# Kernel optimization log

Hardware: AMD Instinct MI355X
Metric: run time of the kernel (lower is better)

Reference implementation:

```python
import jax, jax.numpy as jnp
import numpy as np

NUM_HEADS = 16

def phi(x):
    return jax.nn.elu(x) + 1.0

def setup_inputs() -> dict:
    key = jax.random.key(0)
    ks = jax.random.split(key, 8)
    B, Tq, Tk, H = 4, 8192, 8192, 1024
    s = 1.0 / np.sqrt(H)
    return {
        "q": jax.random.normal(ks[0], (B, Tq, H), jnp.float32),
        "k": jax.random.normal(ks[1], (B, Tk, H), jnp.float32),
        "v": jax.random.normal(ks[2], (B, Tk, H), jnp.float32),
        "mask": jnp.ones((B, Tk), jnp.float32),
        "Wq": jax.random.normal(ks[3], (H, H), jnp.float32) * s,
        "Wk": jax.random.normal(ks[4], (H, H), jnp.float32) * s,
        "Wv": jax.random.normal(ks[5], (H, H), jnp.float32) * s,
        "Wo": jax.random.normal(ks[6], (H, H), jnp.float32) * s,
    }

def reference(q, k, v, mask, Wq, Wk, Wv, Wo):
    B, Tq, H = q.shape
    Tk = k.shape[1]
    nh = NUM_HEADS
    d = H // nh
    # projections (torch Linear: x @ W.T), split heads -> bhtd
    Q = (q @ Wq.T).reshape(B, Tq, nh, d).transpose(0, 2, 1, 3)
    K = (k @ Wk.T).reshape(B, Tk, nh, d).transpose(0, 2, 1, 3)
    V = (v @ Wv.T).reshape(B, Tk, nh, d).transpose(0, 2, 1, 3)
    Q = phi(Q)
    K = phi(K)
    m = mask[:, None, :, None]  # b1t1
    K = K * m
    V = V * m
    K_sum = K.sum(axis=2)                          # bhd
    KV = jnp.einsum('bhtd,bhtv->bhdv', K, V)       # bh d d
    Z = 1.0 / (jnp.einsum('bhtd,bhd->bht', Q, K_sum) + 1e-6)
    out = jnp.einsum('bhtd,bhdv->bhtv', Q, KV) * Z[..., None]
    out = out.transpose(0, 2, 1, 3).reshape(B, Tq, H)
    return out @ Wo.T
```

## Files before the change

### kernel.cpp

```cpp
#include <hip/hip_runtime.h>
#include <hip/hip_bf16.h>
#include <stdint.h>

#define B_  4
#define T_  8192
#define H_  1024
#define NH_ 16
#define D_  64
#define BT_ (B_*T_)

typedef __attribute__((ext_vector_type(8))) __bf16 bf16x8;
typedef __attribute__((ext_vector_type(4))) __bf16 bf16x4;
typedef __attribute__((ext_vector_type(4))) float  f32x4;

__device__ __forceinline__ float phi_f(float x) {
    return x > 0.0f ? x + 1.0f : __expf(x);
}

__device__ __forceinline__ void async_copy16(const void* g, void* l) {
    __builtin_amdgcn_global_load_lds(
        (const __attribute__((address_space(1))) uint32_t*)g,
        (__attribute__((address_space(3))) uint32_t*)l, 16, 0, 0);
}

__global__ void conv_bf16(const float* __restrict__ src, __bf16* __restrict__ dst) {
    size_t i = ((size_t)blockIdx.x * 256 + threadIdx.x) * 8;
    float4 a = *(const float4*)(src + i);
    float4 b = *(const float4*)(src + i + 4);
    bf16x8 o;
    o[0]=(__bf16)a.x; o[1]=(__bf16)a.y; o[2]=(__bf16)a.z; o[3]=(__bf16)a.w;
    o[4]=(__bf16)b.x; o[5]=(__bf16)b.y; o[6]=(__bf16)b.z; o[7]=(__bf16)b.w;
    *(bf16x8*)(dst + i) = o;
}

__global__ void wconv4(const float* __restrict__ s0, const float* __restrict__ s1,
                       const float* __restrict__ s2, const float* __restrict__ s3,
                       __bf16* __restrict__ d0, __bf16* __restrict__ d1,
                       __bf16* __restrict__ d2, __bf16* __restrict__ d3) {
    const float* s; __bf16* d;
    switch (blockIdx.y) {
        case 0: s = s0; d = d0; break;
        case 1: s = s1; d = d1; break;
        case 2: s = s2; d = d2; break;
        default: s = s3; d = d3; break;
    }
    int i = (blockIdx.x * 256 + threadIdx.x) * 4;
    float4 v = *(const float4*)(s + i);
    bf16x4 o;
    o[0] = (__bf16)v.x; o[1] = (__bf16)v.y; o[2] = (__bf16)v.z; o[3] = (__bf16)v.w;
    *(bf16x4*)(d + i) = o;
}

template<int EPI>
__global__ __launch_bounds__(256, 2)
void gemm_bt(const __bf16* __restrict__ A, const __bf16* __restrict__ Wb,
             const float* __restrict__ mask, void* __restrict__ OutV)
{
    const int orig = blockIdx.x;
    const int wgid = (orig & 7) * 256 + (orig >> 3);
    const int bm = (wgid >> 3) * 128;
    const int bn = (wgid & 7) * 128;
    const int tid  = threadIdx.x;
    const int lane = tid & 63;
    const int wid  = tid >> 6;
    const int wm = wid >> 1, wn = wid & 1;

    __shared__ __bf16 Al[128 * 64];
    __shared__ __bf16 Bl[128 * 64];

    f32x4 acc[4][4];
    #pragma unroll
    for (int i = 0; i < 4; ++i)
        #pragma unroll
        for (int j = 0; j < 4; ++j) acc[i][j] = (f32x4)0.0f;

    const int sn = wid * 8 + (lane >> 3);
    const int sc = (lane & 7) * 16;

    for (int k0 = 0; k0 < H_; k0 += 64) {
        #pragma unroll
        for (int issue = 0; issue < 4; ++issue) {
            int n = issue * 32 + sn;
            int csw = sc ^ ((n & 7) << 4);
            async_copy16((const char*)(A  + (size_t)(bm + n) * H_ + k0) + csw,
                         (char*)Al + issue * 4096 + wid * 1024);
            async_copy16((const char*)(Wb + (size_t)(bn + n) * H_ + k0) + csw,
                         (char*)Bl + issue * 4096 + wid * 1024);
        }
        __syncthreads();
        #pragma unroll
        for (int ks = 0; ks < 2; ++ks) {
            bf16x8 afr[4], bfr[4];
            #pragma unroll
            for (int mi = 0; mi < 4; ++mi) {
                int r  = wm * 64 + mi * 16 + (lane & 15);
                int cb = (ks * 64 + (lane >> 4) * 16) ^ ((r & 7) << 4);
                afr[mi] = *(const bf16x8*)((const char*)Al + r * 128 + cb);
            }
            #pragma unroll
            for (int ni = 0; ni < 4; ++ni) {
                int r  = wn * 64 + ni * 16 + (lane & 15);
                int cb = (ks * 64 + (lane >> 4) * 16) ^ ((r & 7) << 4);
                bfr[ni] = *(const bf16x8*)((const char*)Bl + r * 128 + cb);
            }
            #pragma unroll
            for (int mi = 0; mi < 4; ++mi)
                #pragma unroll
                for (int ni = 0; ni < 4; ++ni)
                    acc[mi][ni] = __builtin_amdgcn_mfma_f32_16x16x32_bf16(
                        afr[mi], bfr[ni], acc[mi][ni], 0, 0, 0);
        }
        __syncthreads();
    }
    const int gm0 = bm + wm * 64;
    const int gn0 = bn + wn * 64 + (lane & 15);
    #pragma unroll
    for (int mi = 0; mi < 4; ++mi) {
        #pragma unroll
        for (int j = 0; j < 4; ++j) {
            int gm = gm0 + mi * 16 + (lane >> 4) * 4 + j;
            if (EPI == 3) {
                float* op = (float*)OutV + (size_t)gm * H_ + gn0;
                #pragma unroll
                for (int ni = 0; ni < 4; ++ni)
                    op[ni * 16] = acc[mi][ni][j];
            } else {
                float mv = (EPI >= 1) ? mask[gm] : 1.0f;
                __bf16* op = (__bf16*)OutV + (size_t)gm * H_ + gn0;
                #pragma unroll
                for (int ni = 0; ni < 4; ++ni) {
                    float v = acc[mi][ni][j];
                    if (EPI == 0)      v = phi_f(v);
                    else if (EPI == 1) v = phi_f(v) * mv;
                    else               v = v * mv;
                    op[ni * 16] = (__bf16)v;
                }
            }
        }
    }
}

__global__ __launch_bounds__(256, 2)
void kv_kernel(const __bf16* __restrict__ Kb, const __bf16* __restrict__ Vb,
               float* __restrict__ KVp, float* __restrict__ Ksp)
{
    const int chunk = blockIdx.x;
    const int bh = blockIdx.y;
    const int b = bh >> 4, h = bh & 15;
    const int tid = threadIdx.x, lane = tid & 63, wid = tid >> 6;

    __shared__ char KtRaw[64 * 144];
    __shared__ char VtRaw[64 * 144];
    __shared__ float ksbuf[32][64];

    const int st  = tid >> 3;
    const int dkg = tid & 7;
    const int dk0 = dkg * 8;
    const int swzT = (dkg & 7) << 4;

    f32x4 acc[4];
    #pragma unroll
    for (int i = 0; i < 4; ++i) acc[i] = (f32x4)0.0f;
    float ksacc[8];
    #pragma unroll
    for (int i = 0; i < 8; ++i) ksacc[i] = 0.0f;

    const size_t gbase = ((size_t)b * T_ + (size_t)chunk * 1024) * H_
                         + h * 64 + dk0;

    bf16x8 ka, kc, va, vc;
    {
        const __bf16* p  = Kb + gbase;
        const __bf16* pv = Vb + gbase;
        ka = *(const bf16x8*)(p  + (size_t)st * H_);
        kc = *(const bf16x8*)(p  + (size_t)(st + 32) * H_);
        va = *(const bf16x8*)(pv + (size_t)st * H_);
        vc = *(const bf16x8*)(pv + (size_t)(st + 32) * H_);
    }

    for (int tile = 0; tile < 16; ++tile) {
        __syncthreads();
        #pragma unroll
        for (int j = 0; j < 8; ++j) {
            int rowb = (dk0 + j) * 144;
            *(__bf16*)(KtRaw + ((rowb + 2*st)        ^ swzT)) = ka[j];
            *(__bf16*)(KtRaw + ((rowb + 2*(st + 32)) ^ swzT)) = kc[j];
            *(__bf16*)(VtRaw + ((rowb + 2*st)        ^ swzT)) = va[j];
            *(__bf16*)(VtRaw + ((rowb + 2*(st + 32)) ^ swzT)) = vc[j];
            ksacc[j] += (float)ka[j] + (float)kc[j];
        }
        if (tile < 15) {
            const __bf16* p  = Kb + gbase + (size_t)(tile + 1) * 64 * H_;
            const __bf16* pv = Vb + gbase + (size_t)(tile + 1) * 64 * H_;
            ka = *(const bf16x8*)(p  + (size_t)st * H_);
            kc = *(const bf16x8*)(p  + (size_t)(st + 32) * H_);
            va = *(const bf16x8*)(pv + (size_t)st * H_);
            vc = *(const bf16x8*)(pv + (size_t)(st + 32) * H_);
        }
        __syncthreads();
        #pragma unroll
        for (int ks = 0; ks < 2; ++ks) {
            int r = wid * 16 + (lane & 15);
            int cb = (r * 144 + (ks * 64 + (lane >> 4) * 16)) ^ (((r >> 3) & 7) << 4);
            bf16x8 af = *(const bf16x8*)(KtRaw + cb);
            #pragma unroll
            for (int ni = 0; ni < 4; ++ni) {
                int rv = ni * 16 + (lane & 15);
                int cv = (rv * 144 + (ks * 64 + (lane >> 4) * 16)) ^ (((rv >> 3) & 7) << 4);
                bf16x8 bf = *(const bf16x8*)(VtRaw + cv);
                acc[ni] = __builtin_amdgcn_mfma_f32_16x16x32_bf16(af, bf, acc[ni], 0, 0, 0);
            }
        }
    }

    float* kvp = KVp + ((size_t)chunk * 64 + bh) * 4096;
    #pragma unroll
    for (int ni = 0; ni < 4; ++ni)
        #pragma unroll
        for (int jj = 0; jj < 4; ++jj) {
            int dk = wid * 16 + (lane >> 4) * 4 + jj;
            int dv = ni * 16 + (lane & 15);
            kvp[dk * 64 + dv] = acc[ni][jj];
        }

    #pragma unroll
    for (int j = 0; j < 8; ++j)
        ksbuf[st][dk0 + j] = ksacc[j];
    __syncthreads();
    if (tid < 64) {
        float s = 0.0f;
        #pragma unroll 8
        for (int st2 = 0; st2 < 32; ++st2) s += ksbuf[st2][tid];
        Ksp[((size_t)chunk * 64 + bh) * 64 + tid] = s;
    }
}

__global__ void kvt_kernel(const float* __restrict__ KVp, const float* __restrict__ Ksp,
                           __bf16* __restrict__ KVT, float* __restrict__ Ks) {
    int bh = blockIdx.x, tid = threadIdx.x;
    __bf16* d = KVT + (size_t)bh * 4096;
    for (int i = tid; i < 4096; i += 256) {
        float s = 0.0f;
        #pragma unroll
        for (int c = 0; c < 8; ++c)
            s += KVp[((size_t)c * 64 + bh) * 4096 + i];
        int dk = i >> 6, dv = i & 63;
        d[dv * 64 + dk] = (__bf16)s;
    }
    if (tid < 64) {
        float s = 0.0f;
        #pragma unroll
        for (int c = 0; c < 8; ++c)
            s += Ksp[((size_t)c * 64 + bh) * 64 + tid];
        Ks[bh * 64 + tid] = s;
    }
}

__global__ __launch_bounds__(256, 2)
void attn_kernel(const __bf16* __restrict__ Qb, const __bf16* __restrict__ KVT,
                 const float* __restrict__ Ksum, __bf16* __restrict__ On)
{
    const int bh = blockIdx.y;
    const int b = bh >> 4, h = bh & 15;
    const int tc = blockIdx.x;
    const int tid = threadIdx.x, lane = tid & 63, wid = tid >> 6;
    __shared__ __bf16 kvl[64][72];
    __shared__ float dinv[256];

    {
        const int r = tid >> 2, part = tid & 3;
        const __bf16* src = KVT + (size_t)bh * 4096 + r * 64 + part * 16;
        *(bf16x8*)&kvl[r][part*16]     = *(const bf16x8*)src;
        *(bf16x8*)&kvl[r][part*16 + 8] = *(const bf16x8*)(src + 8);
    }
    {
        const int t = tc * 256 + tid;
        const __bf16* qp = Qb + ((size_t)b * T_ + t) * H_ + h * 64;
        const float* kp = Ksum + bh * 64;
        float s = 0.0f;
        #pragma unroll
        for (int i = 0; i < 8; ++i) {
            bf16x8 qv = *(const bf16x8*)(qp + i * 8);
            #pragma unroll
            for (int j = 0; j < 8; ++j) s += (float)qv[j] * kp[i*8 + j];
        }
        dinv[tid] = 1.0f / (s + 1e-6f);
    }
    __syncthreads();

    f32x4 acc[4][4];
    #pragma unroll
    for (int i = 0; i < 4; ++i)
        #pragma unroll
        for (int j = 0; j < 4; ++j) acc[i][j] = (f32x4)0.0f;

    const int t0 = tc * 256 + wid * 64;
    #pragma unroll
    for (int ks = 0; ks < 2; ++ks) {
        bf16x8 afr[4], bfr[4];
        #pragma unroll
        for (int mi = 0; mi < 4; ++mi) {
            int t = t0 + mi * 16 + (lane & 15);
            afr[mi] = *(const bf16x8*)(Qb + ((size_t)b * T_ + t) * H_ + h * 64
                                       + ks * 32 + (lane >> 4) * 8);
        }
        #pragma unroll
        for (int ni = 0; ni < 4; ++ni) {
            int dv = ni * 16 + (lane & 15);
            bfr[ni] = *(const bf16x8*)&kvl[dv][ks * 32 + (lane >> 4) * 8];
        }
        #pragma unroll
        for (int mi = 0; mi < 4; ++mi)
            #pragma unroll
            for (int ni = 0; ni < 4; ++ni)
                acc[mi][ni] = __builtin_amdgcn_mfma_f32_16x16x32_bf16(
                    afr[mi], bfr[ni], acc[mi][ni], 0, 0, 0);
    }
    #pragma unroll
    for (int mi = 0; mi < 4; ++mi)
        #pragma unroll
        for (int j = 0; j < 4; ++j) {
            int lt = wid * 64 + mi * 16 + (lane >> 4) * 4 + j;
            float z = dinv[lt];
            int t = tc * 256 + lt;
            __bf16* op = On + ((size_t)b * T_ + t) * H_ + h * 64 + (lane & 15);
            #pragma unroll
            for (int ni = 0; ni < 4; ++ni)
                op[ni * 16] = (__bf16)(acc[mi][ni][j] * z);
        }
}

extern "C" void kernel_launch(void* const* d_in, const int* in_sizes, int n_in,
                              void* d_out, int out_size, void* d_ws, size_t ws_size,
                              hipStream_t stream) {
    (void)in_sizes; (void)n_in; (void)out_size; (void)ws_size;
    const float* q    = (const float*)d_in[0];
    const float* k    = (const float*)d_in[1];
    const float* v    = (const float*)d_in[2];
    const float* mask = (const float*)d_in[3];
    const float* Wq   = (const float*)d_in[4];
    const float* Wk   = (const float*)d_in[5];
    const float* Wv   = (const float*)d_in[6];
    const float* Wo   = (const float*)d_in[7];
    float* out = (float*)d_out;

    char* ws = (char*)d_ws;
    const size_t WELEM = (size_t)H_ * H_;
    const size_t PELEM = (size_t)BT_ * H_;
    __bf16* Wqb = (__bf16*)ws;
    __bf16* Wkb = Wqb + WELEM;
    __bf16* Wvb = Wkb + WELEM;
    __bf16* Wob = Wvb + WELEM;
    __bf16* Qb  = Wob + WELEM;
    __bf16* Kb  = Qb + PELEM;
    __bf16* Vb  = Kb + PELEM;
    __bf16* tmp = Vb + PELEM;
    float*  KVp = (float*)(tmp + PELEM);
    float*  Ksp = KVp + (size_t)8 * 64 * 4096;
    float*  Ksf = Ksp + (size_t)8 * 64 * 64;
    __bf16* KVT = (__bf16*)(Ksf + (size_t)64 * 64);

    wconv4<<<dim3(1024, 4), 256, 0, stream>>>(Wq, Wk, Wv, Wo, Wqb, Wkb, Wvb, Wob);

    const int cgrid = (int)(PELEM / (256 * 8));
    conv_bf16<<<cgrid, 256, 0, stream>>>(q, tmp);
    gemm_bt<0><<<2048, 256, 0, stream>>>(tmp, Wqb, mask, Qb);
    conv_bf16<<<cgrid, 256, 0, stream>>>(k, tmp);
    gemm_bt<1><<<2048, 256, 0, stream>>>(tmp, Wkb, mask, Kb);
    conv_bf16<<<cgrid, 256, 0, stream>>>(v, tmp);
    gemm_bt<2><<<2048, 256, 0, stream>>>(tmp, Wvb, mask, Vb);

    kv_kernel<<<dim3(T_/1024, B_*NH_), 256, 0, stream>>>(Kb, Vb, KVp, Ksp);
    kvt_kernel<<<B_*NH_, 256, 0, stream>>>(KVp, Ksp, KVT, Ksf);
    attn_kernel<<<dim3(T_/256, B_*NH_), 256, 0, stream>>>(Qb, KVT, Ksf, tmp);
    gemm_bt<3><<<2048, 256, 0, stream>>>(tmp, Wob, mask, out);
}
```

Measured before the change: 460.7 us.

## Rewrite projection GEMM with 256x256 tiles and 4-stage async LDS pipeline

Replaces the 128x128-tile, single-buffered GEMM with a 256x256 tile using 512 threads (8 waves, each owning 128x64 outputs). A 4-deep ring of 32-wide K slices is staged into 128KB of LDS with direct global-to-LDS loads, and vmcnt-based waits with one barrier per step let loads overlap MFMA work. s_setprio is raised around the MFMA block. The aim is more data reuse per tile and hiding global memory latency, at the cost of large LDS and register use that limits occupancy. The new LDS layout drops the old XOR swizzle, which may bring bank conflicts.

```diff
diff --git a/kernel.cpp b/kernel.cpp
--- a/kernel.cpp
+++ b/kernel.cpp
@@ -52,70 +52,91 @@
 }
 
 template<int EPI>
-__global__ __launch_bounds__(256, 2)
+__global__ __launch_bounds__(512, 2)
 void gemm_bt(const __bf16* __restrict__ A, const __bf16* __restrict__ Wb,
              const float* __restrict__ mask, void* __restrict__ OutV)
 {
+    __shared__ __align__(16) char lds[131072];
+
     const int orig = blockIdx.x;
-    const int wgid = (orig & 7) * 256 + (orig >> 3);
-    const int bm = (wgid >> 3) * 128;
-    const int bn = (wgid & 7) * 128;
-    const int tid  = threadIdx.x;
+    const int wg = (orig & 7) * 64 + (orig >> 3);
+    const int bm = (wg >> 2) * 256;
+    const int bn = (wg & 3) * 256;
+    const int tid = threadIdx.x;
     const int lane = tid & 63;
-    const int wid  = tid >> 6;
-    const int wm = wid >> 1, wn = wid & 1;
-
-    __shared__ __bf16 Al[128 * 64];
-    __shared__ __bf16 Bl[128 * 64];
-
-    f32x4 acc[4][4];
-    #pragma unroll
-    for (int i = 0; i < 4; ++i)
+    const int w = tid >> 6;
+    const int wm = w >> 2, wn = w & 3;
+
+    const int sb0 = w * 1024 + lane * 16;
+    const int sb1 = sb0 + 8192;
+    const int kc0 = sb0 >> 12, row0 = (sb0 & 4095) >> 4;
+    const int kc1 = sb1 >> 12, row1 = (sb1 & 4095) >> 4;
+
+    const __bf16* a0 = A  + (size_t)(bm + row0) * H_ + kc0 * 8;
+    const __bf16* a1 = A  + (size_t)(bm + row1) * H_ + kc1 * 8;
+    const __bf16* b0 = Wb + (size_t)(bn + row0) * H_ + kc0 * 8;
+    const __bf16* b1 = Wb + (size_t)(bn + row1) * H_ + kc1 * 8;
+
+    const int ubA0 = w * 1024;
+    const int ubA1 = ubA0 + 8192;
+
+    const int aoff = (lane >> 4) * 4096 + (lane & 15) * 16 + wm * 2048;
+    const int boff = (lane >> 4) * 4096 + (lane & 15) * 16 + wn * 1024;
+
+    f32x4 acc[8][4];
+    #pragma unroll
+    for (int i = 0; i < 8; ++i)
         #pragma unroll
         for (int j = 0; j < 4; ++j) acc[i][j] = (f32x4)0.0f;
 
-    const int sn = wid * 8 + (lane >> 3);
-    const int sc = (lane & 7) * 16;
-
-    for (int k0 = 0; k0 < H_; k0 += 64) {
-        #pragma unroll
-        for (int issue = 0; issue < 4; ++issue) {
-            int n = issue * 32 + sn;
-            int csw = sc ^ ((n & 7) << 4);
-            async_copy16((const char*)(A  + (size_t)(bm + n) * H_ + k0) + csw,
-                         (char*)Al + issue * 4096 + wid * 1024);
-            async_copy16((const char*)(Wb + (size_t)(bn + n) * H_ + k0) + csw,
-                         (char*)Bl + issue * 4096 + wid * 1024);
-        }
-        __syncthreads();
-        #pragma unroll
-        for (int ks = 0; ks < 2; ++ks) {
-            bf16x8 afr[4], bfr[4];
-            #pragma unroll
-            for (int mi = 0; mi < 4; ++mi) {
-                int r  = wm * 64 + mi * 16 + (lane & 15);
-                int cb = (ks * 64 + (lane >> 4) * 16) ^ ((r & 7) << 4);
-                afr[mi] = *(const bf16x8*)((const char*)Al + r * 128 + cb);
-            }
-            #pragma unroll
-            for (int ni = 0; ni < 4; ++ni) {
-                int r  = wn * 64 + ni * 16 + (lane & 15);
-                int cb = (ks * 64 + (lane >> 4) * 16) ^ ((r & 7) << 4);
-                bfr[ni] = *(const bf16x8*)((const char*)Bl + r * 128 + cb);
-            }
-            #pragma unroll
-            for (int mi = 0; mi < 4; ++mi)
-                #pragma unroll
-                for (int ni = 0; ni < 4; ++ni)
-                    acc[mi][ni] = __builtin_amdgcn_mfma_f32_16x16x32_bf16(
-                        afr[mi], bfr[ni], acc[mi][ni], 0, 0, 0);
-        }
-        __syncthreads();
-    }
-    const int gm0 = bm + wm * 64;
+    auto STAGE = [&](int hh) {
+        const int s_ = (hh & 3) * 16384;
+        const int k_ = hh * 32;
+        async_copy16(a0 + k_, lds + s_ + ubA0);
+        async_copy16(a1 + k_, lds + s_ + ubA1);
+        async_copy16(b0 + k_, lds + 65536 + s_ + ubA0);
+        async_copy16(b1 + k_, lds + 65536 + s_ + ubA1);
+    };
+    auto COMPUTE = [&](int h) {
+        const char* pa = lds + (h & 3) * 16384 + aoff;
+        const char* pb = lds + 65536 + (h & 3) * 16384 + boff;
+        bf16x8 afr[8], bfr[4];
+        #pragma unroll
+        for (int mi = 0; mi < 8; ++mi)
+            afr[mi] = *(const bf16x8*)(pa + mi * 256);
+        #pragma unroll
+        for (int ni = 0; ni < 4; ++ni)
+            bfr[ni] = *(const bf16x8*)(pb + ni * 256);
+        __builtin_amdgcn_s_setprio(1);
+        #pragma unroll
+        for (int mi = 0; mi < 8; ++mi)
+            #pragma unroll
+            for (int ni = 0; ni < 4; ++ni)
+                acc[mi][ni] = __builtin_amdgcn_mfma_f32_16x16x32_bf16(
+                    afr[mi], bfr[ni], acc[mi][ni], 0, 0, 0);
+        __builtin_amdgcn_s_setprio(0);
+    };
+
+    STAGE(0); STAGE(1); STAGE(2);
+
+    #pragma unroll 2
+    for (int h = 0; h < 30; ++h) {
+        asm volatile("s_waitcnt vmcnt(8)" ::: "memory");
+        __builtin_amdgcn_s_barrier();
+        if (h < 29) STAGE(h + 3);
+        COMPUTE(h);
+    }
+    asm volatile("s_waitcnt vmcnt(4)" ::: "memory");
+    __builtin_amdgcn_s_barrier();
+    COMPUTE(30);
+    asm volatile("s_waitcnt vmcnt(0)" ::: "memory");
+    __builtin_amdgcn_s_barrier();
+    COMPUTE(31);
+
+    const int gm0 = bm + wm * 128;
     const int gn0 = bn + wn * 64 + (lane & 15);
     #pragma unroll
-    for (int mi = 0; mi < 4; ++mi) {
+    for (int mi = 0; mi < 8; ++mi) {
         #pragma unroll
         for (int j = 0; j < 4; ++j) {
             int gm = gm0 + mi * 16 + (lane >> 4) * 4 + j;
@@ -363,15 +384,16 @@
     wconv4<<<dim3(1024, 4), 256, 0, stream>>>(Wq, Wk, Wv, Wo, Wqb, Wkb, Wvb, Wob);
 
     const int cgrid = (int)(PELEM / (256 * 8));
+    const int ggrid = (BT_ / 256) * (H_ / 256);
     conv_bf16<<<cgrid, 256, 0, stream>>>(q, tmp);
-    gemm_bt<0><<<2048, 256, 0, stream>>>(tmp, Wqb, mask, Qb);
+    gemm_bt<0><<<ggrid, 512, 0, stream>>>(tmp, Wqb, mask, Qb);
     conv_bf16<<<cgrid, 256, 0, stream>>>(k, tmp);
-    gemm_bt<1><<<2048, 256, 0, stream>>>(tmp, Wkb, mask, Kb);
+    gemm_bt<1><<<ggrid, 512, 0, stream>>>(tmp, Wkb, mask, Kb);
     conv_bf16<<<cgrid, 256, 0, stream>>>(v, tmp);
-    gemm_bt<2><<<2048, 256, 0, stream>>>(tmp, Wvb, mask, Vb);
+    gemm_bt<2><<<ggrid, 512, 0, stream>>>(tmp, Wvb, mask, Vb);
 
     kv_kernel<<<dim3(T_/1024, B_*NH_), 256, 0, stream>>>(Kb, Vb, KVp, Ksp);
     kvt_kernel<<<B_*NH_, 256, 0, stream>>>(KVp, Ksp, KVT, Ksf);
     attn_kernel<<<dim3(T_/256, B_*NH_), 256, 0, stream>>>(Qb, KVT, Ksf, tmp);
-    gemm_bt<3><<<2048, 256, 0, stream>>>(tmp, Wob, mask, out);
-}
+    gemm_bt<3><<<ggrid, 512, 0, stream>>>(tmp, Wob, mask, out);
+}
```

Measured after the change: 626.1 us. +35.9%, slower.

## Fold KV state into output projection and fuse normalizer into Q projection

Applied to the files above, without the earlier changes.

Reassociates the linear-attention output so that per-batch matrices Wo·KV are precomputed by a small GEMM, and the final projection reads phi(Q)·Z directly with per-batch weights. The attention kernel, its extra read of Q and write of the attention output are removed, and the Z normalizer is computed in the Q-projection epilogue with lane shuffles. Costs are a per-batch weight buffer (4x the Wo size) that the last GEMM must stream, and an extra bf16 rounding at a different point in the computation.

```diff
diff --git a/kernel.cpp b/kernel.cpp
--- a/kernel.cpp
+++ b/kernel.cpp
@@ -54,7 +54,8 @@
 template<int EPI>
 __global__ __launch_bounds__(256, 2)
 void gemm_bt(const __bf16* __restrict__ A, const __bf16* __restrict__ Wb,
-             const float* __restrict__ mask, void* __restrict__ OutV)
+             const float* __restrict__ mask, const float* __restrict__ aux,
+             void* __restrict__ OutV)
 {
     const int orig = blockIdx.x;
     const int wgid = (orig & 7) * 256 + (orig >> 3);
@@ -65,6 +66,9 @@
     const int wid  = tid >> 6;
     const int wm = wid >> 1, wn = wid & 1;
 
+    const __bf16* Wp = Wb;
+    if (EPI == 3) Wp = Wb + ((size_t)(bm >> 13) << 20);
+
     __shared__ __bf16 Al[128 * 64];
     __shared__ __bf16 Bl[128 * 64];
 
@@ -84,7 +88,7 @@
             int csw = sc ^ ((n & 7) << 4);
             async_copy16((const char*)(A  + (size_t)(bm + n) * H_ + k0) + csw,
                          (char*)Al + issue * 4096 + wid * 1024);
-            async_copy16((const char*)(Wb + (size_t)(bn + n) * H_ + k0) + csw,
+            async_copy16((const char*)(Wp + (size_t)(bn + n) * H_ + k0) + csw,
                          (char*)Bl + issue * 4096 + wid * 1024);
         }
         __syncthreads();
@@ -114,26 +118,57 @@
     }
     const int gm0 = bm + wm * 64;
     const int gn0 = bn + wn * 64 + (lane & 15);
-    #pragma unroll
-    for (int mi = 0; mi < 4; ++mi) {
-        #pragma unroll
-        for (int j = 0; j < 4; ++j) {
-            int gm = gm0 + mi * 16 + (lane >> 4) * 4 + j;
-            if (EPI == 3) {
-                float* op = (float*)OutV + (size_t)gm * H_ + gn0;
+
+    if (EPI == 0) {
+        const int b = bm >> 13;
+        const int h = (bn >> 6) + wn;
+        float ksv[4];
+        #pragma unroll
+        for (int ni = 0; ni < 4; ++ni)
+            ksv[ni] = aux[((b * 16 + h) << 6) + ni * 16 + (lane & 15)];
+        #pragma unroll
+        for (int mi = 0; mi < 4; ++mi) {
+            #pragma unroll
+            for (int j = 0; j < 4; ++j) {
+                float pv[4], s = 0.0f;
+                #pragma unroll
+                for (int ni = 0; ni < 4; ++ni) {
+                    pv[ni] = phi_f(acc[mi][ni][j]);
+                    s += pv[ni] * ksv[ni];
+                }
+                s += __shfl_xor(s, 1);
+                s += __shfl_xor(s, 2);
+                s += __shfl_xor(s, 4);
+                s += __shfl_xor(s, 8);
+                float z = 1.0f / (s + 1e-6f);
+                int gm = gm0 + mi * 16 + (lane >> 4) * 4 + j;
+                __bf16* op = (__bf16*)OutV + (size_t)gm * H_ + gn0;
                 #pragma unroll
                 for (int ni = 0; ni < 4; ++ni)
-                    op[ni * 16] = acc[mi][ni][j];
-            } else {
-                float mv = (EPI >= 1) ? mask[gm] : 1.0f;
-                __bf16* op = (__bf16*)OutV + (size_t)gm * H_ + gn0;
-                #pragma unroll
-                for (int ni = 0; ni < 4; ++ni) {
-                    float v = acc[mi][ni][j];
-                    if (EPI == 0)      v = phi_f(v);
-                    else if (EPI == 1) v = phi_f(v) * mv;
-                    else               v = v * mv;
-                    op[ni * 16] = (__bf16)v;
+                    op[ni * 16] = (__bf16)(pv[ni] * z);
+            }
+        }
+    } else {
+        #pragma unroll
+        for (int mi = 0; mi < 4; ++mi) {
+            #pragma unroll
+            for (int j = 0; j < 4; ++j) {
+                int gm = gm0 + mi * 16 + (lane >> 4) * 4 + j;
+                if (EPI == 3) {
+                    float* op = (float*)OutV + (size_t)gm * H_ + gn0;
+                    #pragma unroll
+                    for (int ni = 0; ni < 4; ++ni)
+                        op[ni * 16] = acc[mi][ni][j];
+                } else {
+                    float mv = mask[gm];
+                    __bf16* op = (__bf16*)OutV + (size_t)gm * H_ + gn0;
+                    #pragma unroll
+                    for (int ni = 0; ni < 4; ++ni) {
+                        float v = acc[mi][ni][j];
+                        if (EPI == 1) v = phi_f(v) * mv;
+                        else          v = v * mv;
+                        op[ni * 16] = (__bf16)v;
+                    }
                 }
             }
         }
@@ -235,17 +270,16 @@
     }
 }
 
-__global__ void kvt_kernel(const float* __restrict__ KVp, const float* __restrict__ Ksp,
-                           __bf16* __restrict__ KVT, float* __restrict__ Ks) {
+__global__ void kvsum(const float* __restrict__ KVp, const float* __restrict__ Ksp,
+                      __bf16* __restrict__ KVb, float* __restrict__ Ks) {
     int bh = blockIdx.x, tid = threadIdx.x;
-    __bf16* d = KVT + (size_t)bh * 4096;
+    __bf16* d = KVb + (size_t)bh * 4096;
     for (int i = tid; i < 4096; i += 256) {
         float s = 0.0f;
         #pragma unroll
         for (int c = 0; c < 8; ++c)
             s += KVp[((size_t)c * 64 + bh) * 4096 + i];
-        int dk = i >> 6, dv = i & 63;
-        d[dv * 64 + dk] = (__bf16)s;
+        d[i] = (__bf16)s;
     }
     if (tid < 64) {
         float s = 0.0f;
@@ -256,35 +290,34 @@
     }
 }
 
-__global__ __launch_bounds__(256, 2)
-void attn_kernel(const __bf16* __restrict__ Qb, const __bf16* __restrict__ KVT,
-                 const float* __restrict__ Ksum, __bf16* __restrict__ On)
+__global__ __launch_bounds__(256)
+void ugemm(const __bf16* __restrict__ Wob, const __bf16* __restrict__ KVb,
+           __bf16* __restrict__ Ut)
 {
-    const int bh = blockIdx.y;
-    const int b = bh >> 4, h = bh & 15;
-    const int tc = blockIdx.x;
-    const int tid = threadIdx.x, lane = tid & 63, wid = tid >> 6;
-    __shared__ __bf16 kvl[64][72];
-    __shared__ float dinv[256];
+    const int mp = blockIdx.x, bhp = blockIdx.y;
+    const int b = bhp >> 3, hp = bhp & 7;
+    const int tid = threadIdx.x, lane = tid & 63, w = tid >> 6;
+    const int wm = w >> 1, wn = w & 1;
+    const int h = hp * 2 + wn;
+    const int bm = mp * 128;
+    const int lane15 = lane & 15;
+
+    __shared__ __bf16 As[128][136];
+    __shared__ __bf16 Bs[2][64][72];
 
     {
-        const int r = tid >> 2, part = tid & 3;
-        const __bf16* src = KVT + (size_t)bh * 4096 + r * 64 + part * 16;
-        *(bf16x8*)&kvl[r][part*16]     = *(const bf16x8*)src;
-        *(bf16x8*)&kvl[r][part*16 + 8] = *(const bf16x8*)(src + 8);
+        int r = tid >> 1, c0 = (tid & 1) * 64;
+        const __bf16* src = Wob + (size_t)(bm + r) * H_ + hp * 128 + c0;
+        #pragma unroll
+        for (int j = 0; j < 8; ++j)
+            *(bf16x8*)&As[r][c0 + j*8] = *(const bf16x8*)(src + j*8);
     }
     {
-        const int t = tc * 256 + tid;
-        const __bf16* qp = Qb + ((size_t)b * T_ + t) * H_ + h * 64;
-        const float* kp = Ksum + bh * 64;
-        float s = 0.0f;
-        #pragma unroll
-        for (int i = 0; i < 8; ++i) {
-            bf16x8 qv = *(const bf16x8*)(qp + i * 8);
-            #pragma unroll
-            for (int j = 0; j < 8; ++j) s += (float)qv[j] * kp[i*8 + j];
-        }
-        dinv[tid] = 1.0f / (s + 1e-6f);
+        int hh = tid >> 7, idx = tid & 127, r = idx >> 1, c0 = (idx & 1) * 32;
+        const __bf16* src = KVb + ((size_t)(b * 16 + hp * 2 + hh) * 64 + r) * 64 + c0;
+        #pragma unroll
+        for (int j = 0; j < 4; ++j)
+            *(bf16x8*)&Bs[hh][r][c0 + j*8] = *(const bf16x8*)(src + j*8);
     }
     __syncthreads();
 
@@ -294,21 +327,17 @@
         #pragma unroll
         for (int j = 0; j < 4; ++j) acc[i][j] = (f32x4)0.0f;
 
-    const int t0 = tc * 256 + wid * 64;
     #pragma unroll
     for (int ks = 0; ks < 2; ++ks) {
         bf16x8 afr[4], bfr[4];
         #pragma unroll
-        for (int mi = 0; mi < 4; ++mi) {
-            int t = t0 + mi * 16 + (lane & 15);
-            afr[mi] = *(const bf16x8*)(Qb + ((size_t)b * T_ + t) * H_ + h * 64
-                                       + ks * 32 + (lane >> 4) * 8);
-        }
-        #pragma unroll
-        for (int ni = 0; ni < 4; ++ni) {
-            int dv = ni * 16 + (lane & 15);
-            bfr[ni] = *(const bf16x8*)&kvl[dv][ks * 32 + (lane >> 4) * 8];
-        }
+        for (int mi = 0; mi < 4; ++mi)
+            afr[mi] = *(const bf16x8*)&As[wm*64 + mi*16 + lane15]
+                                         [wn*64 + ks*32 + (lane>>4)*8];
+        #pragma unroll
+        for (int ni = 0; ni < 4; ++ni)
+            bfr[ni] = *(const bf16x8*)&Bs[wn][ni*16 + lane15]
+                                         [ks*32 + (lane>>4)*8];
         #pragma unroll
         for (int mi = 0; mi < 4; ++mi)
             #pragma unroll
@@ -316,17 +345,18 @@
                 acc[mi][ni] = __builtin_amdgcn_mfma_f32_16x16x32_bf16(
                     afr[mi], bfr[ni], acc[mi][ni], 0, 0, 0);
     }
+
+    __bf16* up = Ut + ((size_t)b << 20);
     #pragma unroll
     for (int mi = 0; mi < 4; ++mi)
         #pragma unroll
         for (int j = 0; j < 4; ++j) {
-            int lt = wid * 64 + mi * 16 + (lane >> 4) * 4 + j;
-            float z = dinv[lt];
-            int t = tc * 256 + lt;
-            __bf16* op = On + ((size_t)b * T_ + t) * H_ + h * 64 + (lane & 15);
-            #pragma unroll
-            for (int ni = 0; ni < 4; ++ni)
-                op[ni * 16] = (__bf16)(acc[mi][ni][j] * z);
+            int m2 = bm + wm * 64 + mi * 16 + (lane >> 4) * 4 + j;
+            #pragma unroll
+            for (int ni = 0; ni < 4; ++ni) {
+                int dk = ni * 16 + lane15;
+                up[(size_t)m2 * H_ + h * 64 + dk] = (__bf16)acc[mi][ni][j];
+            }
         }
 }
 
@@ -358,20 +388,22 @@
     float*  KVp = (float*)(tmp + PELEM);
     float*  Ksp = KVp + (size_t)8 * 64 * 4096;
     float*  Ksf = Ksp + (size_t)8 * 64 * 64;
-    __bf16* KVT = (__bf16*)(Ksf + (size_t)64 * 64);
+    __bf16* KVb = (__bf16*)(Ksf + (size_t)64 * 64);
+    __bf16* Ut  = (__bf16*)KVp;
 
     wconv4<<<dim3(1024, 4), 256, 0, stream>>>(Wq, Wk, Wv, Wo, Wqb, Wkb, Wvb, Wob);
 
     const int cgrid = (int)(PELEM / (256 * 8));
+    conv_bf16<<<cgrid, 256, 0, stream>>>(k, tmp);
+    gemm_bt<1><<<2048, 256, 0, stream>>>(tmp, Wkb, mask, nullptr, Kb);
+    conv_bf16<<<cgrid, 256, 0, stream>>>(v, tmp);
+    gemm_bt<2><<<2048, 256, 0, stream>>>(tmp, Wvb, mask, nullptr, Vb);
+
+    kv_kernel<<<dim3(T_/1024, B_*NH_), 256, 0, stream>>>(Kb, Vb, KVp, Ksp);
+    kvsum<<<B_*NH_, 256, 0, stream>>>(KVp, Ksp, KVb, Ksf);
+    ugemm<<<dim3(8, 32), 256, 0, stream>>>(Wob, KVb, Ut);
+
     conv_bf16<<<cgrid, 256, 0, stream>>>(q, tmp);
-    gemm_bt<0><<<2048, 256, 0, stream>>>(tmp, Wqb, mask, Qb);
-    conv_bf16<<<cgrid, 256, 0, stream>>>(k, tmp);
-    gemm_bt<1><<<2048, 256, 0, stream>>>(tmp, Wkb, mask, Kb);
-    conv_bf16<<<cgrid, 256, 0, stream>>>(v, tmp);
-    gemm_bt<2><<<2048, 256, 0, stream>>>(tmp, Wvb, mask, Vb);
-
-    kv_kernel<<<dim3(T_/1024, B_*NH_), 256, 0, stream>>>(Kb, Vb, KVp, Ksp);
-    kvt_kernel<<<B_*NH_, 256, 0, stream>>>(KVp, Ksp, KVT, Ksf);
-    attn_kernel<<<dim3(T_/256, B_*NH_), 256, 0, stream>>>(Qb, KVT, Ksf, tmp);
-    gemm_bt<3><<<2048, 256, 0, stream>>>(tmp, Wob, mask, out);
-}
+    gemm_bt<0><<<2048, 256, 0, stream>>>(tmp, Wqb, mask, Ksf, Qb);
+    gemm_bt<3><<<2048, 256, 0, stream>>>(Qb, (const __bf16*)Ut, mask, nullptr, out);
+}
```

Result: faster. 431.7 us (-6.3%).
